# Performance work log

Measured on AMD Instinct MI355X. Metric: run time of the kernel, lower is better.

The kernel has to match this reference:

```python
import jax, jax.numpy as jnp
import numpy as np

P = 16          # num_points (knots per piecewise-linear function)
LO, HI = -1.0, 1.0  # uniform knot grid range
EPS = 1e-6


def apl(x, v):
    """Adaptive piecewise-linear layer on a uniform grid.
    x: (N, I), v: (I, P, O) learnable knot values. out[n,o] = sum_i interp_i(x[n,i])."""
    I, Pk, O = v.shape
    t = (jnp.clip(x, LO, HI) - LO) / (HI - LO) * (Pk - 1)   # (N, I) in [0, P-1]
    idx = jnp.clip(jnp.floor(t), 0, Pk - 2).astype(jnp.int32)
    frac = t - idx
    ar = jnp.arange(Pk)
    # sparse interpolation weights (N, I, P): two nonzeros per (n, i)
    w = (jnp.where(ar == idx[..., None], (1.0 - frac)[..., None], 0.0)
         + jnp.where(ar == idx[..., None] + 1, frac[..., None], 0.0))
    return jnp.einsum('nip,ipo->no', w, v)


def max_abs_normalize(h):
    B, T, D = h.shape
    hn = h.reshape(B * T, D)
    hn = hn / (jnp.max(jnp.abs(hn), axis=1, keepdims=True) + EPS)
    return hn.reshape(B, T, D)


def mingru_layer(x, h0, vz, vh):
    """x: (B,T,Din), h0: (B,D). Returns normalized hidden states (B,T,D)."""
    B, T, _ = x.shape
    xf = x.reshape(B * T, -1)
    h_bar = apl(xf, vh).reshape(B, T, -1)
    z = jax.nn.sigmoid(apl(xf, vz)).reshape(B, T, -1)
    a = 1.0 - z
    b = z * h_bar
    # unstable closed-form recurrence: h[t] = A[t] * (h0 + cumsum(b/A))
    A = jnp.cumprod(a, axis=1)
    S = jnp.cumsum(b / A, axis=1)
    h = A * (h0[:, None, :] + S)
    return max_abs_normalize(h)


def setup_inputs() -> dict:
    key = jax.random.key(0)
    ks = jax.random.split(key, 8)
    B, T, Din, D, Dout = 8, 2048, 64, 64, 64
    Z_OFF = -6.0 / Din  # bias z-layer output to ~-6 so sigmoid(z) is small -> cumprod stays finite
    x = jax.random.normal(ks[0], (B, T, Din), dtype=jnp.float32)
    def vz(k, I, O):
        return 0.05 * jax.random.normal(k, (I, P, O), dtype=jnp.float32) + Z_OFF
    def vh(k, I, O):
        return 0.5 * jax.random.normal(k, (I, P, O), dtype=jnp.float32)
    return {
        'x': x,
        'vz0': vz(ks[1], Din, D), 'vh0': vh(ks[2], Din, D),
        'vz1': vz(ks[3], D, D),   'vh1': vh(ks[4], D, D),
        'vz2': vz(ks[5], D, D),   'vh2': vh(ks[6], D, D),
        'vout': 0.5 * jax.random.normal(ks[7], (D, P, Dout), dtype=jnp.float32),
    }


def reference(x, vz0, vh0, vz1, vh1, vz2, vh2, vout):
    B, T, _ = x.shape
    D = vh0.shape[-1]
    h0 = jnp.zeros((B, D), dtype=x.dtype)
    cur = mingru_layer(x, h0, vz0, vh0)
    cur = mingru_layer(cur, h0, vz1, vh1)
    cur = mingru_layer(cur, h0, vz2, vh2)
    out = apl(cur.reshape(B * T, -1), vout).reshape(B, T, -1)
    return out
```

## Files before the change

kernel.cpp:

```cpp
#include <hip/hip_runtime.h>


#define WPB 8
#define NC 64
#define CL 32

__global__ __launch_bounds__(256) void prep_dual_kernel(
    const float* __restrict__ vz, const float* __restrict__ vh,
    float4* __restrict__ tab)
{
    int idx = blockIdx.x * blockDim.x + threadIdx.x;
    if (idx >= 64 * 15 * 64) return;
    int o = idx & 63;
    int p = (idx >> 6) % 15;
    int i = idx / (15 * 64);
    int base = (i * 16 + p) * 64 + o;
    float z0 = vz[base], z1 = vz[base + 64];
    float h0 = vh[base], h1 = vh[base + 64];
    tab[idx] = make_float4(z0, z1 - z0, h0, h1 - h0);
}

__global__ __launch_bounds__(256) void prep_out_kernel(
    const float* __restrict__ v, float2* __restrict__ tab)
{
    int idx = blockIdx.x * blockDim.x + threadIdx.x;
    if (idx >= 64 * 15 * 64) return;
    int o = idx & 63;
    int p = (idx >> 6) % 15;
    int i = idx / (15 * 64);
    int base = (i * 16 + p) * 64 + o;
    float v0 = v[base], v1 = v[base + 64];
    tab[idx] = make_float2(v0, v1 - v0);
}

__global__ __launch_bounds__(512) void apl_dual_kernel(
    const float* __restrict__ in, const float4* __restrict__ tab,
    float2* __restrict__ zh, int N)
{
    const int lane = threadIdx.x & 63;
    const int n = blockIdx.x * WPB + (threadIdx.x >> 6);
    if (n >= N) return;

    float xv = in[(size_t)n * 64 + lane];
    float tv = fminf(fmaxf(xv, -1.f), 1.f) * 7.5f + 7.5f;
    int iv = (int)tv; iv = iv > 14 ? 14 : iv;
    float frv = tv - (float)iv;
    int offv = lane * 15360 + (iv << 10);

    const char* tb = (const char*)tab + lane * 16;
    float accz0 = 0.f, acch0 = 0.f, accz1 = 0.f, acch1 = 0.f;
#pragma unroll
    for (int i0 = 0; i0 < 64; i0 += 4) {
        int of0 = __shfl(offv, i0 + 0, 64);
        int of1 = __shfl(offv, i0 + 1, 64);
        int of2 = __shfl(offv, i0 + 2, 64);
        int of3 = __shfl(offv, i0 + 3, 64);
        float fr0 = __shfl(frv, i0 + 0, 64);
        float fr1 = __shfl(frv, i0 + 1, 64);
        float fr2 = __shfl(frv, i0 + 2, 64);
        float fr3 = __shfl(frv, i0 + 3, 64);
        float4 e0 = *(const float4*)(tb + of0);
        float4 e1 = *(const float4*)(tb + of1);
        float4 e2 = *(const float4*)(tb + of2);
        float4 e3 = *(const float4*)(tb + of3);
        accz0 += fmaf(fr0, e0.y, e0.x);
        acch0 += fmaf(fr0, e0.w, e0.z);
        accz1 += fmaf(fr1, e1.y, e1.x);
        acch1 += fmaf(fr1, e1.w, e1.z);
        accz0 += fmaf(fr2, e2.y, e2.x);
        acch0 += fmaf(fr2, e2.w, e2.z);
        accz1 += fmaf(fr3, e3.y, e3.x);
        acch1 += fmaf(fr3, e3.w, e3.z);
    }
    float accz = accz0 + accz1, acch = acch0 + acch1;
    float z = 1.f / (1.f + expf(-accz));
    zh[(size_t)n * 64 + lane] = make_float2(z, acch);
}

__global__ __launch_bounds__(512) void apl_out_kernel(
    const float* __restrict__ in, const float2* __restrict__ tab,
    float* __restrict__ out, int N)
{
    const int lane = threadIdx.x & 63;
    const int n = blockIdx.x * WPB + (threadIdx.x >> 6);
    if (n >= N) return;

    float xv = in[(size_t)n * 64 + lane];
    float tv = fminf(fmaxf(xv, -1.f), 1.f) * 7.5f + 7.5f;
    int iv = (int)tv; iv = iv > 14 ? 14 : iv;
    float frv = tv - (float)iv;
    int offv = lane * 7680 + (iv << 9);

    const char* tb = (const char*)tab + lane * 8;
    float acc0 = 0.f, acc1 = 0.f;
#pragma unroll
    for (int i0 = 0; i0 < 64; i0 += 8) {
        int of[8]; float fr[8]; float2 e[8];
#pragma unroll
        for (int j = 0; j < 8; ++j) of[j] = __shfl(offv, i0 + j, 64);
#pragma unroll
        for (int j = 0; j < 8; ++j) fr[j] = __shfl(frv, i0 + j, 64);
#pragma unroll
        for (int j = 0; j < 8; ++j) e[j] = *(const float2*)(tb + of[j]);
#pragma unroll
        for (int j = 0; j < 8; j += 2) {
            acc0 += fmaf(fr[j], e[j].y, e[j].x);
            acc1 += fmaf(fr[j + 1], e[j + 1].y, e[j + 1].x);
        }
    }
    out[(size_t)n * 64 + lane] = acc0 + acc1;
}

__global__ __launch_bounds__(256) void scan_pass1_kernel(
    const float2* __restrict__ zh, float2* __restrict__ chunkAB, int T)
{
    int lane = threadIdx.x & 63;
    int wid = blockIdx.x * (blockDim.x >> 6) + (threadIdx.x >> 6);
    int b = wid / NC, c = wid % NC;
    const float2* p = zh + ((size_t)b * T + (size_t)c * CL) * 64 + lane;

    float A = 1.f, Bc = 0.f;
    for (int k0 = 0; k0 < CL; k0 += 8) {
        float2 v[8];
#pragma unroll
        for (int k = 0; k < 8; ++k) v[k] = p[(size_t)(k0 + k) * 64];
#pragma unroll
        for (int k = 0; k < 8; ++k) {
            float a = 1.f - v[k].x;
            float bb = v[k].x * v[k].y;
            A *= a;
            Bc = fmaf(a, Bc, bb);
        }
    }
    chunkAB[(size_t)wid * 64 + lane] = make_float2(A, Bc);
}

__global__ __launch_bounds__(64) void scan_fixup_kernel(
    const float2* __restrict__ chunkAB, float* __restrict__ hinit)
{
    int b = blockIdx.x;
    int d = threadIdx.x;
    const float2* p = chunkAB + (size_t)b * NC * 64 + d;
    float* o = hinit + (size_t)b * NC * 64 + d;

    float h = 0.f;
    for (int c0 = 0; c0 < NC; c0 += 8) {
        float2 ab[8];
#pragma unroll
        for (int k = 0; k < 8; ++k) ab[k] = p[(size_t)(c0 + k) * 64];
#pragma unroll
        for (int k = 0; k < 8; ++k) {
            o[(size_t)(c0 + k) * 64] = h;
            h = fmaf(ab[k].x, h, ab[k].y);
        }
    }
}

__global__ __launch_bounds__(256) void scan_pass2_kernel(
    const float2* __restrict__ zh, const float* __restrict__ hinit,
    float* __restrict__ out, int T)
{
    int lane = threadIdx.x & 63;
    int wid = blockIdx.x * (blockDim.x >> 6) + (threadIdx.x >> 6);
    int b = wid / NC, c = wid % NC;
    const float2* p = zh + ((size_t)b * T + (size_t)c * CL) * 64 + lane;
    float* o = out + ((size_t)b * T + (size_t)c * CL) * 64 + lane;

    float h = hinit[(size_t)wid * 64 + lane];
    for (int k0 = 0; k0 < CL; k0 += 8) {
        float2 v[8];
        float hs[8];
#pragma unroll
        for (int k = 0; k < 8; ++k) v[k] = p[(size_t)(k0 + k) * 64];
#pragma unroll
        for (int k = 0; k < 8; ++k) {
            h = fmaf(v[k].x, v[k].y - h, h);
            hs[k] = h;
        }
#pragma unroll
        for (int k = 0; k < 8; ++k) {
            float m = fabsf(hs[k]);
            m = fmaxf(m, __shfl_xor(m, 32, 64));
            m = fmaxf(m, __shfl_xor(m, 16, 64));
            m = fmaxf(m, __shfl_xor(m, 8, 64));
            m = fmaxf(m, __shfl_xor(m, 4, 64));
            m = fmaxf(m, __shfl_xor(m, 2, 64));
            m = fmaxf(m, __shfl_xor(m, 1, 64));
            o[(size_t)(k0 + k) * 64] = hs[k] / (m + 1e-6f);
        }
    }
}

extern "C" void kernel_launch(void* const* d_in, const int* in_sizes, int n_in,
                              void* d_out, int out_size, void* d_ws, size_t ws_size,
                              hipStream_t stream) {
    const float* x    = (const float*)d_in[0];
    const float* vz0  = (const float*)d_in[1];
    const float* vh0  = (const float*)d_in[2];
    const float* vz1  = (const float*)d_in[3];
    const float* vh1  = (const float*)d_in[4];
    const float* vz2  = (const float*)d_in[5];
    const float* vh2  = (const float*)d_in[6];
    const float* vout = (const float*)d_in[7];

    const int N = in_sizes[0] / 64;
    const int T = NC * CL;
    const int B = N / T;

    char* ws = (char*)d_ws;
    const size_t TAB_ELEMS = (size_t)64 * 15 * 64;
    float2* zh      = (float2*)ws;
    float*  cur     = (float*)(ws + 8388608);
    float4* tab0    = (float4*)(ws + 12582912);
    float4* tab1    = (float4*)(ws + 13565952);
    float4* tab2    = (float4*)(ws + 14548992);
    float2* tab_out = (float2*)(ws + 15532032);
    float2* chunkAB = (float2*)(ws + 16023552);
    float*  hinit   = (float*)(ws + 16285696);

    dim3 pblk(256), pgrd((TAB_ELEMS + 255) / 256);
    prep_dual_kernel<<<pgrd, pblk, 0, stream>>>(vz0, vh0, tab0);
    prep_dual_kernel<<<pgrd, pblk, 0, stream>>>(vz1, vh1, tab1);
    prep_dual_kernel<<<pgrd, pblk, 0, stream>>>(vz2, vh2, tab2);
    prep_out_kernel<<<pgrd, pblk, 0, stream>>>(vout, tab_out);

    dim3 ablk(64 * WPB), agrd((N + WPB - 1) / WPB);
    dim3 sblk(256), sgrd(B * NC / 4);

    const float4* tabs[3] = {tab0, tab1, tab2};
    const float* layer_in = x;
    for (int l = 0; l < 3; ++l) {
        apl_dual_kernel<<<agrd, ablk, 0, stream>>>(layer_in, tabs[l], zh, N);
        scan_pass1_kernel<<<sgrd, sblk, 0, stream>>>(zh, chunkAB, T);
        scan_fixup_kernel<<<B, 64, 0, stream>>>(chunkAB, hinit);
        scan_pass2_kernel<<<sgrd, sblk, 0, stream>>>(zh, hinit, cur, T);
        layer_in = cur;
    }
    apl_out_kernel<<<agrd, ablk, 0, stream>>>(cur, tab_out, (float*)d_out, N);
}
```

Measured before the change: 192.0 us.

## Fuse chunk scan reduction into APL kernel and drop fixup kernel

The APL dual kernel now emits (a, b) pairs instead of (z, h_bar). Each 16-row block reduces its chunk's (A, B) carry through shared memory, replacing the separate scan_pass1 kernel. The fixup kernel is removed: each pass2 wave serially recomposes the prefix carry from all earlier chunk summaries. Launches per layer drop from four to two, at the cost of redundant prefix work in pass2 (up to 127 chunk loads per wave) and larger 1024-thread blocks.

```diff
diff --git a/kernel.cpp b/kernel.cpp
--- a/kernel.cpp
+++ b/kernel.cpp
@@ -1,9 +1,9 @@
 #include <hip/hip_runtime.h>
 
 
-#define WPB 8
-#define NC 64
-#define CL 32
+#define WPB 16
+#define CL  16
+#define NCB (2048 / CL)
 
 __global__ __launch_bounds__(256) void prep_dual_kernel(
     const float* __restrict__ vz, const float* __restrict__ vh,
@@ -33,13 +33,15 @@
     tab[idx] = make_float2(v0, v1 - v0);
 }
 
-__global__ __launch_bounds__(512) void apl_dual_kernel(
+__global__ __launch_bounds__(1024) void apl_dual_kernel(
     const float* __restrict__ in, const float4* __restrict__ tab,
-    float2* __restrict__ zh, int N)
+    float2* __restrict__ zh, float2* __restrict__ chunkAB)
 {
     const int lane = threadIdx.x & 63;
-    const int n = blockIdx.x * WPB + (threadIdx.x >> 6);
-    if (n >= N) return;
+    const int w = threadIdx.x >> 6;
+    const int n = blockIdx.x * WPB + w;
+
+    __shared__ float2 ab_lds[WPB][64];
 
     float xv = in[(size_t)n * 64 + lane];
     float tv = fminf(fmaxf(xv, -1.f), 1.f) * 7.5f + 7.5f;
@@ -74,16 +76,30 @@
     }
     float accz = accz0 + accz1, acch = acch0 + acch1;
     float z = 1.f / (1.f + expf(-accz));
-    zh[(size_t)n * 64 + lane] = make_float2(z, acch);
-}
-
-__global__ __launch_bounds__(512) void apl_out_kernel(
+    float a = 1.f - z;
+    float bb = z * acch;
+    zh[(size_t)n * 64 + lane] = make_float2(a, bb);
+    ab_lds[w][lane] = make_float2(a, bb);
+    __syncthreads();
+
+    if (w == 0) {
+        float A = 1.f, Bc = 0.f;
+#pragma unroll
+        for (int k = 0; k < WPB; ++k) {
+            float2 t = ab_lds[k][lane];
+            A = t.x * A;
+            Bc = fmaf(t.x, Bc, t.y);
+        }
+        chunkAB[(size_t)blockIdx.x * 64 + lane] = make_float2(A, Bc);
+    }
+}
+
+__global__ __launch_bounds__(1024) void apl_out_kernel(
     const float* __restrict__ in, const float2* __restrict__ tab,
-    float* __restrict__ out, int N)
+    float* __restrict__ out)
 {
     const int lane = threadIdx.x & 63;
     const int n = blockIdx.x * WPB + (threadIdx.x >> 6);
-    if (n >= N) return;
 
     float xv = in[(size_t)n * 64 + lane];
     float tv = fminf(fmaxf(xv, -1.f), 1.f) * 7.5f + 7.5f;
@@ -111,62 +127,28 @@
     out[(size_t)n * 64 + lane] = acc0 + acc1;
 }
 
-__global__ __launch_bounds__(256) void scan_pass1_kernel(
-    const float2* __restrict__ zh, float2* __restrict__ chunkAB, int T)
-{
-    int lane = threadIdx.x & 63;
-    int wid = blockIdx.x * (blockDim.x >> 6) + (threadIdx.x >> 6);
-    int b = wid / NC, c = wid % NC;
-    const float2* p = zh + ((size_t)b * T + (size_t)c * CL) * 64 + lane;
-
-    float A = 1.f, Bc = 0.f;
-    for (int k0 = 0; k0 < CL; k0 += 8) {
-        float2 v[8];
-#pragma unroll
-        for (int k = 0; k < 8; ++k) v[k] = p[(size_t)(k0 + k) * 64];
-#pragma unroll
-        for (int k = 0; k < 8; ++k) {
-            float a = 1.f - v[k].x;
-            float bb = v[k].x * v[k].y;
-            A *= a;
-            Bc = fmaf(a, Bc, bb);
-        }
-    }
-    chunkAB[(size_t)wid * 64 + lane] = make_float2(A, Bc);
-}
-
-__global__ __launch_bounds__(64) void scan_fixup_kernel(
-    const float2* __restrict__ chunkAB, float* __restrict__ hinit)
-{
-    int b = blockIdx.x;
-    int d = threadIdx.x;
-    const float2* p = chunkAB + (size_t)b * NC * 64 + d;
-    float* o = hinit + (size_t)b * NC * 64 + d;
-
+__global__ __launch_bounds__(256) void scan_pass2_kernel(
+    const float2* __restrict__ zh, const float2* __restrict__ chunkAB,
+    float* __restrict__ out, int T)
+{
+    const int lane = threadIdx.x & 63;
+    const int wid = blockIdx.x * 4 + (threadIdx.x >> 6);
+    const int b = wid / NCB, c = wid % NCB;
+
+    const float2* pc = chunkAB + ((size_t)b * NCB) * 64 + lane;
     float h = 0.f;
-    for (int c0 = 0; c0 < NC; c0 += 8) {
+    int j = 0;
+    for (; j + 8 <= c; j += 8) {
         float2 ab[8];
 #pragma unroll
-        for (int k = 0; k < 8; ++k) ab[k] = p[(size_t)(c0 + k) * 64];
-#pragma unroll
-        for (int k = 0; k < 8; ++k) {
-            o[(size_t)(c0 + k) * 64] = h;
-            h = fmaf(ab[k].x, h, ab[k].y);
-        }
-    }
-}
-
-__global__ __launch_bounds__(256) void scan_pass2_kernel(
-    const float2* __restrict__ zh, const float* __restrict__ hinit,
-    float* __restrict__ out, int T)
-{
-    int lane = threadIdx.x & 63;
-    int wid = blockIdx.x * (blockDim.x >> 6) + (threadIdx.x >> 6);
-    int b = wid / NC, c = wid % NC;
+        for (int k = 0; k < 8; ++k) ab[k] = pc[(size_t)(j + k) * 64];
+#pragma unroll
+        for (int k = 0; k < 8; ++k) h = fmaf(ab[k].x, h, ab[k].y);
+    }
+    for (; j < c; ++j) { float2 ab = pc[(size_t)j * 64]; h = fmaf(ab.x, h, ab.y); }
+
     const float2* p = zh + ((size_t)b * T + (size_t)c * CL) * 64 + lane;
     float* o = out + ((size_t)b * T + (size_t)c * CL) * 64 + lane;
-
-    float h = hinit[(size_t)wid * 64 + lane];
     for (int k0 = 0; k0 < CL; k0 += 8) {
         float2 v[8];
         float hs[8];
@@ -174,7 +156,7 @@
         for (int k = 0; k < 8; ++k) v[k] = p[(size_t)(k0 + k) * 64];
 #pragma unroll
         for (int k = 0; k < 8; ++k) {
-            h = fmaf(v[k].x, v[k].y - h, h);
+            h = fmaf(v[k].x, h, v[k].y);
             hs[k] = h;
         }
 #pragma unroll
@@ -204,7 +186,7 @@
     const float* vout = (const float*)d_in[7];
 
     const int N = in_sizes[0] / 64;
-    const int T = NC * CL;
+    const int T = 2048;
     const int B = N / T;
 
     char* ws = (char*)d_ws;
@@ -216,7 +198,6 @@
     float4* tab2    = (float4*)(ws + 14548992);
     float2* tab_out = (float2*)(ws + 15532032);
     float2* chunkAB = (float2*)(ws + 16023552);
-    float*  hinit   = (float*)(ws + 16285696);
 
     dim3 pblk(256), pgrd((TAB_ELEMS + 255) / 256);
     prep_dual_kernel<<<pgrd, pblk, 0, stream>>>(vz0, vh0, tab0);
@@ -224,17 +205,15 @@
     prep_dual_kernel<<<pgrd, pblk, 0, stream>>>(vz2, vh2, tab2);
     prep_out_kernel<<<pgrd, pblk, 0, stream>>>(vout, tab_out);
 
-    dim3 ablk(64 * WPB), agrd((N + WPB - 1) / WPB);
-    dim3 sblk(256), sgrd(B * NC / 4);
+    dim3 ablk(64 * WPB), agrd(N / WPB);
+    dim3 sblk(256), sgrd(B * NCB / 4);
 
     const float4* tabs[3] = {tab0, tab1, tab2};
     const float* layer_in = x;
     for (int l = 0; l < 3; ++l) {
-        apl_dual_kernel<<<agrd, ablk, 0, stream>>>(layer_in, tabs[l], zh, N);
-        scan_pass1_kernel<<<sgrd, sblk, 0, stream>>>(zh, chunkAB, T);
-        scan_fixup_kernel<<<B, 64, 0, stream>>>(chunkAB, hinit);
-        scan_pass2_kernel<<<sgrd, sblk, 0, stream>>>(zh, hinit, cur, T);
+        apl_dual_kernel<<<agrd, ablk, 0, stream>>>(layer_in, tabs[l], zh, chunkAB);
+        scan_pass2_kernel<<<sgrd, sblk, 0, stream>>>(zh, chunkAB, cur, T);
         layer_in = cur;
     }
-    apl_out_kernel<<<agrd, ablk, 0, stream>>>(cur, tab_out, (float*)d_out, N);
-}
+    apl_out_kernel<<<agrd, ablk, 0, stream>>>(cur, tab_out, (float*)d_out);
+}
```

Measured after the change: 196.4 us. 1.02x slower.
